# Optimization experiments

Hardware: AMD Instinct MI355X
Metric: run time of the kernel (lower is better)

Reference implementation:

```python
import jax, jax.numpy as jnp
import numpy as np

N_HEAD = 12

def setup_inputs() -> dict:
    key = jax.random.key(0)
    k1, k2, k3 = jax.random.split(key, 3)
    B, T, C = 2, 4096, 768
    x = jax.random.normal(k1, (B, T, C), dtype=jnp.float32)
    Wqkv = jax.random.normal(k2, (C, 3 * C), dtype=jnp.float32) * (1.0 / np.sqrt(C))
    bqkv = jnp.zeros((3 * C,), dtype=jnp.float32)
    Wout = jax.random.normal(k3, (C, C), dtype=jnp.float32) * (1.0 / np.sqrt(C))
    bout = jnp.zeros((C,), dtype=jnp.float32)
    return {"x": x, "Wqkv": Wqkv, "bqkv": bqkv, "Wout": Wout, "bout": bout}

def reference(x, Wqkv, bqkv, Wout, bout):
    B, T, C = x.shape
    H = N_HEAD
    D = C // H
    qkv = x @ Wqkv + bqkv                       # [B,T,3C]
    qkv = qkv.reshape(B, T, 3, H, D)
    q = qkv[:, :, 0].transpose(0, 2, 1, 3)       # [B,H,T,D]
    k = qkv[:, :, 1].transpose(0, 2, 1, 3)
    v = qkv[:, :, 2].transpose(0, 2, 1, 3)
    att = jnp.einsum('bhqd,bhkd->bhqk', q, k) / jnp.sqrt(jnp.float32(D))
    causal = jnp.tril(jnp.ones((T, T), dtype=bool))
    att = jnp.where(causal[None, None], att, jnp.float32(-jnp.inf))
    att = jax.nn.softmax(att, axis=-1)
    out = jnp.einsum('bhqk,bhkd->bhqd', att, v)  # [B,H,T,D]
    out = out.transpose(0, 2, 1, 3).reshape(B, T, C)
    return out @ Wout + bout
```

## Files before the change

### kernel.cpp

```cpp
#include <hip/hip_runtime.h>
#include <math.h>

#define Bb 2
#define Tt 4096
#define Cc 768
#define Hh 12
#define Dd 64

typedef __attribute__((ext_vector_type(8))) short short8;
typedef __attribute__((ext_vector_type(4))) float f32x4;
typedef __attribute__((ext_vector_type(4))) unsigned short u16x4;

static __device__ __forceinline__ unsigned short f2bf(float f) {
    unsigned u = __float_as_uint(f);
    u += 0x7FFF + ((u >> 16) & 1);
    return (unsigned short)(u >> 16);
}

static __device__ __forceinline__ float ex2(float x) {
    return __builtin_amdgcn_exp2f(x);
}

static __device__ __forceinline__ void gload16(const void* g, void* l) {
    __builtin_amdgcn_global_load_lds(
        (const __attribute__((address_space(1))) unsigned*)g,
        (__attribute__((address_space(3))) unsigned*)l, 16, 0, 0);
}

__global__ __launch_bounds__(256)
void cvt_bf16(const float* __restrict__ in, unsigned short* __restrict__ out, int n8) {
    int i = blockIdx.x * 256 + threadIdx.x;
    if (i >= n8) return;
    float4 a = *(const float4*)(in + (size_t)i * 8);
    float4 b = *(const float4*)(in + (size_t)i * 8 + 4);
    union { short8 v; unsigned short u[8]; } p;
    p.u[0] = f2bf(a.x); p.u[1] = f2bf(a.y); p.u[2] = f2bf(a.z); p.u[3] = f2bf(a.w);
    p.u[4] = f2bf(b.x); p.u[5] = f2bf(b.y); p.u[6] = f2bf(b.z); p.u[7] = f2bf(b.w);
    *(short8*)(out + (size_t)i * 8) = p.v;
}

__global__ __launch_bounds__(256)
void transpose_w(const float* __restrict__ W, unsigned short* __restrict__ Wt,
                 int K, int N) {
    __shared__ __align__(16) unsigned short Tl[64][72];
    int n0 = blockIdx.x * 64, k0 = blockIdx.y * 64;
    int t = threadIdx.x;
    int r = t >> 2, c = (t & 3) * 16;
    const float* wp = W + (size_t)(k0 + r) * N + n0 + c;
    #pragma unroll
    for (int j = 0; j < 16; j += 4) {
        float4 v = *(const float4*)(wp + j);
        Tl[c + j + 0][r] = f2bf(v.x);
        Tl[c + j + 1][r] = f2bf(v.y);
        Tl[c + j + 2][r] = f2bf(v.z);
        Tl[c + j + 3][r] = f2bf(v.w);
    }
    __syncthreads();
    unsigned short* op = Wt + (size_t)(n0 + r) * K + k0 + c;
    *(short8*)op       = *(const short8*)&Tl[r][c];
    *(short8*)(op + 8) = *(const short8*)&Tl[r][c + 8];
}

__global__ __launch_bounds__(256)
void repack_vt(const unsigned short* __restrict__ qkvb, unsigned short* __restrict__ vtb) {
    __shared__ __align__(16) unsigned short Tl[64][72];
    int t0 = blockIdx.x * 64, h = blockIdx.y, b = blockIdx.z;
    int t = threadIdx.x;
    int r = t >> 2, c = (t & 3) * 16;
    const unsigned short* vp = qkvb + (size_t)((size_t)b * Tt + t0 + r) * (3 * Cc)
                               + 2 * Cc + h * Dd + c;
    short8 v0 = *(const short8*)vp;
    short8 v1 = *(const short8*)(vp + 8);
    #pragma unroll
    for (int j = 0; j < 8; ++j) {
        Tl[c + j][r]     = ((unsigned short*)&v0)[j];
        Tl[c + 8 + j][r] = ((unsigned short*)&v1)[j];
    }
    __syncthreads();
    unsigned short* op = vtb + ((size_t)((b * Hh + h) * Dd) + r) * Tt + t0 + c;
    *(short8*)op       = *(const short8*)&Tl[r][c];
    *(short8*)(op + 8) = *(const short8*)&Tl[r][c + 8];
}

template<bool BF16OUT>
__global__ __launch_bounds__(256)
void gemm_mfma(const unsigned short* __restrict__ A, const unsigned short* __restrict__ Bt,
               const float* __restrict__ bias, void* __restrict__ Cout,
               int M, int N, int K, int qcols) {
    __shared__ __align__(16) unsigned short As[128][64];
    __shared__ __align__(16) unsigned short Bs[128][64];
    const int tid = threadIdx.x;
    const int wid = tid >> 6, lane = tid & 63;
    const int lr = lane & 15, g = lane >> 4;
    const int wr = wid >> 1, wc = wid & 1;
    const int m0 = blockIdx.y * 128, n0 = blockIdx.x * 128;
    const int srow = lane >> 3;
    const int scol = (lane & 7) * 8;

    f32x4 acc[4][4] = {};

    for (int k0 = 0; k0 < K; k0 += 64) {
        #pragma unroll
        for (int j = 0; j < 4; ++j) {
            int ci = wid * 4 + j;
            int row = ci * 8 + srow;
            gload16(A  + (size_t)(m0 + row) * K + k0 + scol, &As[ci * 8][0]);
            gload16(Bt + (size_t)(n0 + row) * K + k0 + scol, &Bs[ci * 8][0]);
        }
        __syncthreads();
        #pragma unroll
        for (int ks = 0; ks < 2; ++ks) {
            short8 af[4], bfr[4];
            #pragma unroll
            for (int m = 0; m < 4; ++m)
                af[m] = *(const short8*)&As[wr * 64 + m * 16 + lr][ks * 32 + g * 8];
            #pragma unroll
            for (int n = 0; n < 4; ++n)
                bfr[n] = *(const short8*)&Bs[wc * 64 + n * 16 + lr][ks * 32 + g * 8];
            #pragma unroll
            for (int m = 0; m < 4; ++m)
                #pragma unroll
                for (int n = 0; n < 4; ++n)
                    acc[m][n] = __builtin_amdgcn_mfma_f32_16x16x32_bf16(
                        af[m], bfr[n], acc[m][n], 0, 0, 0);
        }
        __syncthreads();
    }

    const float qscale = 0.125f * 1.44269504088896340736f;
    #pragma unroll
    for (int n = 0; n < 4; ++n) {
        int coln = n0 + wc * 64 + n * 16 + lr;
        float bv = bias[coln];
        float sc = (coln < qcols) ? qscale : 1.0f;
        #pragma unroll
        for (int m = 0; m < 4; ++m) {
            int rowb = m0 + wr * 64 + m * 16 + g * 4;
            #pragma unroll
            for (int r = 0; r < 4; ++r) {
                float v = (acc[m][n][r] + bv) * sc;
                if (BF16OUT)
                    ((unsigned short*)Cout)[(size_t)(rowb + r) * N + coln] = f2bf(v);
                else
                    ((float*)Cout)[(size_t)(rowb + r) * N + coln] = v;
            }
        }
    }
}

__global__ __launch_bounds__(256)
void attn_mfma(const unsigned short* __restrict__ qkvb,
               const unsigned short* __restrict__ vtb,
               unsigned short* __restrict__ outb) {
    const int P  = blockIdx.x;
    const int hd = blockIdx.y, b = blockIdx.z;
    const int tid = threadIdx.x;
    const int wid = tid >> 6, lane = tid & 63;
    const int lr = lane & 15, g = lane >> 4;
    const int rm7 = lr & 7;
    const size_t rs = 3 * Cc;

    __shared__ __align__(16) unsigned short Ks[2][64 * 64];
    __shared__ __align__(16) unsigned short Vs[2][64 * 64];

    const unsigned short* qkvbase = qkvb + (size_t)b * Tt * rs;
    const unsigned short* vbase   = vtb + (size_t)((b * Hh + hd) * Dd) * Tt;

    const int srw  = lane >> 3;
    const int row0 = wid * 8 + srw;
    const int slog = (lane & 7) ^ (srw & 7);
    const unsigned short* ksrc0 = qkvbase + (size_t)row0 * rs + Cc + hd * Dd + slog * 8;
    const unsigned short* vsrc0 = vbase + (size_t)row0 * Tt + slog * 8;

    const int ntA = 64 - P;
    const int ntB = P + 1;

    auto stage = [&](int buf, int t) {
        gload16(ksrc0 + (size_t)t * 64 * rs,        &Ks[buf][wid * 512]);
        gload16(ksrc0 + (size_t)(t * 64 + 32) * rs, &Ks[buf][2048 + wid * 512]);
        gload16(vsrc0 + t * 64,                     &Vs[buf][wid * 512]);
        gload16(vsrc0 + (size_t)32 * Tt + t * 64,   &Vs[buf][2048 + wid * 512]);
    };

    stage(0, 0);
    __syncthreads();
    int cur = 0;

    const int laneA = lr + ((g & 1) << 5);
    const int laneB = laneA + 16;
    const int asel  = g >> 1;

    #pragma unroll 1
    for (int pass = 0; pass < 2; ++pass) {
        const int q0  = (pass ? P : 63 - P) * 64;
        const int nt  = pass ? ntB : ntA;
        const int myq = q0 + wid * 16 + lr;

        short8 qf0, qf1;
        {
            const unsigned short* qp = qkvbase + (size_t)myq * rs + hd * Dd;
            qf0 = *(const short8*)(qp + g * 8);
            qf1 = *(const short8*)(qp + 32 + g * 8);
        }

        f32x4 o[4];
        #pragma unroll
        for (int dt = 0; dt < 4; ++dt) o[dt] = (f32x4){0.f, 0.f, 0.f, 0.f};
        float m_r = -1e30f, l_r = 0.f;

        #pragma unroll 1
        for (int kbt = 0; kbt < nt; ++kbt) {
            if (kbt + 1 < nt)       stage(cur ^ 1, kbt + 1);
            else if (pass == 0)     stage(cur ^ 1, 0);

            const unsigned short* Kc = &Ks[cur][0];
            const unsigned short* Vc = &Vs[cur][0];

            f32x4 st[4];
            __builtin_amdgcn_s_setprio(1);
            #pragma unroll
            for (int kt = 0; kt < 4; ++kt) {
                int row = kt * 16 + lr;
                int off0 = row * 64 + (g ^ rm7) * 8;
                short8 kf0 = *(const short8*)&Kc[off0];
                short8 kf1 = *(const short8*)&Kc[off0 ^ 32];
                f32x4 a = (f32x4){0.f, 0.f, 0.f, 0.f};
                a = __builtin_amdgcn_mfma_f32_16x16x32_bf16(kf0, qf0, a, 0, 0, 0);
                a = __builtin_amdgcn_mfma_f32_16x16x32_bf16(kf1, qf1, a, 0, 0, 0);
                st[kt] = a;
            }
            __builtin_amdgcn_s_setprio(0);

            if (kbt == nt - 1) {
                #pragma unroll
                for (int kt = 0; kt < 4; ++kt)
                    #pragma unroll
                    for (int r = 0; r < 4; ++r)
                        if (kbt * 64 + kt * 16 + g * 4 + r > myq) st[kt][r] = -1e30f;
            }

            float tmax = -1e30f;
            #pragma unroll
            for (int kt = 0; kt < 4; ++kt)
                #pragma unroll
                for (int r = 0; r < 4; ++r) tmax = fmaxf(tmax, st[kt][r]);
            tmax = fmaxf(tmax, __shfl_xor(tmax, 16));
            tmax = fmaxf(tmax, __shfl_xor(tmax, 32));
            if (!__all(tmax - m_r <= 8.0f)) {
                float mnew = fmaxf(m_r, tmax);
                float corr = ex2(m_r - mnew);
                l_r *= corr;
                #pragma unroll
                for (int dt = 0; dt < 4; ++dt)
                    #pragma unroll
                    for (int r = 0; r < 4; ++r) o[dt][r] *= corr;
                m_r = mnew;
            }
            float psum = 0.f;
            #pragma unroll
            for (int kt = 0; kt < 4; ++kt)
                #pragma unroll
                for (int r = 0; r < 4; ++r) {
                    float p = ex2(st[kt][r] - m_r);
                    st[kt][r] = p;
                    psum += p;
                }
            psum += __shfl_xor(psum, 16);
            psum += __shfl_xor(psum, 32);
            l_r += psum;

            unsigned up[4][2];
            #pragma unroll
            for (int kt = 0; kt < 4; ++kt) {
                asm("v_cvt_pk_bf16_f32 %0, %1, %2"
                    : "=v"(up[kt][0]) : "v"(st[kt][0]), "v"(st[kt][1]));
                asm("v_cvt_pk_bf16_f32 %0, %1, %2"
                    : "=v"(up[kt][1]) : "v"(st[kt][2]), "v"(st[kt][3]));
            }
            #pragma unroll
            for (int ks = 0; ks < 2; ++ks) {
                unsigned wa0 = __shfl(up[2 * ks][0],     laneA);
                unsigned wb0 = __shfl(up[2 * ks + 1][0], laneA);
                unsigned wa1 = __shfl(up[2 * ks][1],     laneA);
                unsigned wb1 = __shfl(up[2 * ks + 1][1], laneA);
                unsigned wa2 = __shfl(up[2 * ks][0],     laneB);
                unsigned wb2 = __shfl(up[2 * ks + 1][0], laneB);
                unsigned wa3 = __shfl(up[2 * ks][1],     laneB);
                unsigned wb3 = __shfl(up[2 * ks + 1][1], laneB);
                union { unsigned w[4]; short8 v; } pb;
                pb.w[0] = asel ? wb0 : wa0;
                pb.w[1] = asel ? wb1 : wa1;
                pb.w[2] = asel ? wb2 : wa2;
                pb.w[3] = asel ? wb3 : wa3;
                __builtin_amdgcn_s_setprio(1);
                #pragma unroll
                for (int dt = 0; dt < 4; ++dt) {
                    int row = dt * 16 + lr;
                    int off = row * 64 + (((ks << 2) | g) ^ rm7) * 8;
                    short8 vf = *(const short8*)&Vc[off];
                    o[dt] = __builtin_amdgcn_mfma_f32_16x16x32_bf16(vf, pb.v, o[dt], 0, 0, 0);
                }
                __builtin_amdgcn_s_setprio(0);
            }

            __syncthreads();
            cur ^= 1;
        }

        float inv = 1.f / fmaxf(l_r, 1e-37f);
        unsigned short* op = outb + ((size_t)b * Tt + myq) * Cc + hd * Dd + g * 4;
        #pragma unroll
        for (int dt = 0; dt < 4; ++dt) {
            u16x4 w;
            #pragma unroll
            for (int r = 0; r < 4; ++r) w[r] = f2bf(o[dt][r] * inv);
            *(u16x4*)(op + dt * 16) = w;
        }
    }
}

extern "C" void kernel_launch(void* const* d_in, const int* in_sizes, int n_in,
                              void* d_out, int out_size, void* d_ws, size_t ws_size,
                              hipStream_t stream) {
    const float* x    = (const float*)d_in[0];
    const float* Wqkv = (const float*)d_in[1];
    const float* bqkv = (const float*)d_in[2];
    const float* Wout = (const float*)d_in[3];
    const float* bout = (const float*)d_in[4];
    float* out = (float*)d_out;

    const int M = Bb * Tt;
    const int N1 = 3 * Cc;

    char* p = (char*)d_ws;
    unsigned short* qkvb  = (unsigned short*)p; p += (size_t)M * N1 * 2;
    unsigned short* xb    = (unsigned short*)p; p += (size_t)M * Cc * 2;
    unsigned short* wqkvt = (unsigned short*)p; p += (size_t)N1 * Cc * 2;
    unsigned short* woutt = (unsigned short*)p; p += (size_t)Cc * Cc * 2;
    unsigned short* vtb   = (unsigned short*)p; p += (size_t)Bb * Hh * Dd * Tt * 2;
    unsigned short* attb  = (unsigned short*)p; p += (size_t)M * Cc * 2;

    cvt_bf16<<<dim3((M * Cc / 8 + 255) / 256), dim3(256), 0, stream>>>(x, xb, M * Cc / 8);
    transpose_w<<<dim3(N1 / 64, Cc / 64), dim3(256), 0, stream>>>(Wqkv, wqkvt, Cc, N1);
    transpose_w<<<dim3(Cc / 64, Cc / 64), dim3(256), 0, stream>>>(Wout, woutt, Cc, Cc);

    gemm_mfma<true><<<dim3(N1 / 128, M / 128), dim3(256), 0, stream>>>(
        xb, wqkvt, bqkv, qkvb, M, N1, Cc, Cc);

    repack_vt<<<dim3(Tt / 64, Hh, Bb), dim3(256), 0, stream>>>(qkvb, vtb);

    attn_mfma<<<dim3(Tt / 128, Hh, Bb), dim3(256), 0, stream>>>(qkvb, vtb, attb);

    gemm_mfma<false><<<dim3(Cc / 128, M / 128), dim3(256), 0, stream>>>(
        attb, woutt, bout, out, M, Cc, Cc, 0);
}
```

Before: 222.9 us.

## Fuse V transpose into QKV GEMM epilogue and remap attention blocks per XCD

The QKV GEMM epilogue now handles the V column tiles itself: it transposes them through shared memory (a union reusing the A/B tile buffers) and writes V^T directly. This removes the separate repack_vt kernel and its extra read and write of V. The V tiles no longer write V into qkvb, which is fine because attention reads V from vtb. Attention now launches as a 1D grid, decoding blockIdx so that the blocks for each (batch, head) pair land on the same XCD, with the aim of better L2 reuse of K/V.

```diff
diff --git a/kernel.cpp b/kernel.cpp
--- a/kernel.cpp
+++ b/kernel.cpp
@@ -61,34 +61,17 @@
     *(short8*)(op + 8) = *(const short8*)&Tl[r][c + 8];
 }
 
-__global__ __launch_bounds__(256)
-void repack_vt(const unsigned short* __restrict__ qkvb, unsigned short* __restrict__ vtb) {
-    __shared__ __align__(16) unsigned short Tl[64][72];
-    int t0 = blockIdx.x * 64, h = blockIdx.y, b = blockIdx.z;
-    int t = threadIdx.x;
-    int r = t >> 2, c = (t & 3) * 16;
-    const unsigned short* vp = qkvb + (size_t)((size_t)b * Tt + t0 + r) * (3 * Cc)
-                               + 2 * Cc + h * Dd + c;
-    short8 v0 = *(const short8*)vp;
-    short8 v1 = *(const short8*)(vp + 8);
-    #pragma unroll
-    for (int j = 0; j < 8; ++j) {
-        Tl[c + j][r]     = ((unsigned short*)&v0)[j];
-        Tl[c + 8 + j][r] = ((unsigned short*)&v1)[j];
-    }
-    __syncthreads();
-    unsigned short* op = vtb + ((size_t)((b * Hh + h) * Dd) + r) * Tt + t0 + c;
-    *(short8*)op       = *(const short8*)&Tl[r][c];
-    *(short8*)(op + 8) = *(const short8*)&Tl[r][c + 8];
-}
-
 template<bool BF16OUT>
 __global__ __launch_bounds__(256)
 void gemm_mfma(const unsigned short* __restrict__ A, const unsigned short* __restrict__ Bt,
                const float* __restrict__ bias, void* __restrict__ Cout,
-               int M, int N, int K, int qcols) {
-    __shared__ __align__(16) unsigned short As[128][64];
-    __shared__ __align__(16) unsigned short Bs[128][64];
+               int M, int N, int K, int qcols,
+               unsigned short* __restrict__ vtb, int voff) {
+    union SmemU {
+        unsigned short ab[2][128][64];
+        unsigned short tv[128][136];
+    };
+    __shared__ __align__(16) SmemU sh;
     const int tid = threadIdx.x;
     const int wid = tid >> 6, lane = tid & 63;
     const int lr = lane & 15, g = lane >> 4;
@@ -104,8 +87,8 @@
         for (int j = 0; j < 4; ++j) {
             int ci = wid * 4 + j;
             int row = ci * 8 + srow;
-            gload16(A  + (size_t)(m0 + row) * K + k0 + scol, &As[ci * 8][0]);
-            gload16(Bt + (size_t)(n0 + row) * K + k0 + scol, &Bs[ci * 8][0]);
+            gload16(A  + (size_t)(m0 + row) * K + k0 + scol, &sh.ab[0][ci * 8][0]);
+            gload16(Bt + (size_t)(n0 + row) * K + k0 + scol, &sh.ab[1][ci * 8][0]);
         }
         __syncthreads();
         #pragma unroll
@@ -113,10 +96,10 @@
             short8 af[4], bfr[4];
             #pragma unroll
             for (int m = 0; m < 4; ++m)
-                af[m] = *(const short8*)&As[wr * 64 + m * 16 + lr][ks * 32 + g * 8];
+                af[m] = *(const short8*)&sh.ab[0][wr * 64 + m * 16 + lr][ks * 32 + g * 8];
             #pragma unroll
             for (int n = 0; n < 4; ++n)
-                bfr[n] = *(const short8*)&Bs[wc * 64 + n * 16 + lr][ks * 32 + g * 8];
+                bfr[n] = *(const short8*)&sh.ab[1][wc * 64 + n * 16 + lr][ks * 32 + g * 8];
             #pragma unroll
             for (int m = 0; m < 4; ++m)
                 #pragma unroll
@@ -125,6 +108,36 @@
                         af[m], bfr[n], acc[m][n], 0, 0, 0);
         }
         __syncthreads();
+    }
+
+    if (vtb != nullptr && n0 >= voff) {
+        #pragma unroll
+        for (int n = 0; n < 4; ++n) {
+            int tcol = wc * 64 + n * 16 + lr;
+            float bv = bias[n0 + tcol];
+            #pragma unroll
+            for (int m = 0; m < 4; ++m) {
+                int trow = wr * 64 + m * 16 + g * 4;
+                #pragma unroll
+                for (int r = 0; r < 4; ++r)
+                    sh.tv[tcol][trow + r] = f2bf(acc[m][n][r] + bv);
+            }
+        }
+        __syncthreads();
+        const int dlocal = tid >> 1;
+        const int th     = (tid & 1) * 64;
+        const int colg   = n0 + dlocal;
+        const int hd     = (colg - voff) >> 6;
+        const int d      = (colg - voff) & 63;
+        const int token  = m0 + th;
+        const int bq     = token >> 12;
+        const int t0     = token & (Tt - 1);
+        unsigned short* dst = vtb + ((size_t)(bq * Hh + hd) * Dd + d) * Tt + t0;
+        const unsigned short* src = &sh.tv[dlocal][th];
+        #pragma unroll
+        for (int j = 0; j < 8; ++j)
+            *(short8*)(dst + j * 8) = *(const short8*)(src + j * 8);
+        return;
     }
 
     const float qscale = 0.125f * 1.44269504088896340736f;
@@ -152,8 +165,13 @@
 void attn_mfma(const unsigned short* __restrict__ qkvb,
                const unsigned short* __restrict__ vtb,
                unsigned short* __restrict__ outb) {
-    const int P  = blockIdx.x;
-    const int hd = blockIdx.y, b = blockIdx.z;
+    const int nid  = blockIdx.x;
+    const int xcd  = nid & 7;
+    const int rest = nid >> 3;
+    const int P    = rest & 31;
+    const int H2   = xcd + 8 * (rest >> 5);
+    const int hd   = H2 % Hh;
+    const int b    = H2 / Hh;
     const int tid = threadIdx.x;
     const int wid = tid >> 6, lane = tid & 63;
     const int lr = lane & 15, g = lane >> 4;
@@ -345,12 +363,10 @@
     transpose_w<<<dim3(Cc / 64, Cc / 64), dim3(256), 0, stream>>>(Wout, woutt, Cc, Cc);
 
     gemm_mfma<true><<<dim3(N1 / 128, M / 128), dim3(256), 0, stream>>>(
-        xb, wqkvt, bqkv, qkvb, M, N1, Cc, Cc);
-
-    repack_vt<<<dim3(Tt / 64, Hh, Bb), dim3(256), 0, stream>>>(qkvb, vtb);
-
-    attn_mfma<<<dim3(Tt / 128, Hh, Bb), dim3(256), 0, stream>>>(qkvb, vtb, attb);
+        xb, wqkvt, bqkv, qkvb, M, N1, Cc, Cc, vtb, 2 * Cc);
+
+    attn_mfma<<<dim3(32 * Hh * Bb), dim3(256), 0, stream>>>(qkvb, vtb, attb);
 
     gemm_mfma<false><<<dim3(Cc / 128, M / 128), dim3(256), 0, stream>>>(
-        attb, woutt, bout, out, M, Cc, Cc, 0);
-}
+        attb, woutt, bout, out, M, Cc, Cc, 0, nullptr, 1 << 30);
+}
```

After: 212.9 us. 4.5% less time.
